# Optimization experiments

Hardware: AMD Instinct MI355X
Metric: run time of the kernel (lower is better)

The kernel has to match this reference:

```python
import jax, jax.numpy as jnp
import numpy as np

VAR_FLOOR = 0.002
BS, A, IN, H, L, NNH, ATT, NACT = 1024, 32, 96, 64, 16, 64, 32, 16


def _lin(x, w, b):
    return x @ w.T + b


def _lrelu(x):
    return jax.nn.leaky_relu(x, 0.01)


def setup_inputs() -> dict:
    key = jax.random.key(0)
    ks = jax.random.split(key, 24)
    def w(k, o, i):
        return jax.random.normal(k, (o, i), jnp.float32) / np.float32(np.sqrt(i))
    def b(k, o):
        return jax.random.normal(k, (o,), jnp.float32) * 0.01
    N = BS * A
    return {
        "inputs": jax.random.normal(ks[0], (N, IN), jnp.float32),
        "hidden_state": jax.random.normal(ks[1], (N, H), jnp.float32),
        "eps": jax.random.normal(ks[2], (N, A * L), jnp.float32),
        "fc1_w": w(ks[3], H, IN), "fc1_b": b(ks[4], H),
        "gru_wih": w(ks[5], 3 * H, H), "gru_whh": w(ks[6], 3 * H, H),
        "gru_bih": b(ks[7], 3 * H), "gru_bhh": b(ks[8], 3 * H),
        "fc2_w": w(ks[9], NACT, H), "fc2_b": b(ks[10], NACT),
        "emb_w1": w(ks[11], NNH, H), "emb_b1": b(ks[12], NNH),
        "bn_g": jnp.ones((NNH,), jnp.float32), "bn_b": jnp.zeros((NNH,), jnp.float32),
        "emb_w2": w(ks[13], A * L * 2, NNH), "emb_b2": b(ks[14], A * L * 2),
        "msg_w1": w(ks[15], NNH, H + L), "msg_b1": b(ks[16], NNH),
        "msg_w2": w(ks[17], NACT, NNH), "msg_b2": b(ks[18], NACT),
        "wq_w": w(ks[19], ATT, H), "wq_b": b(ks[20], ATT),
        "wk_w": w(ks[21], ATT, L), "wk_b": b(ks[22], ATT),
        "bs": BS, "t": 0,
    }


def reference(inputs, hidden_state, eps, fc1_w, fc1_b, gru_wih, gru_whh, gru_bih,
              gru_bhh, fc2_w, fc2_b, emb_w1, emb_b1, bn_g, bn_b, emb_w2, emb_b2,
              msg_w1, msg_b1, msg_w2, msg_b2, wq_w, wq_b, wk_w, wk_b, bs, t):
    Hd = fc1_w.shape[0]
    x = jax.nn.relu(_lin(inputs, fc1_w, fc1_b))
    h_in = hidden_state.reshape(-1, Hd)
    # GRUCell
    gi = _lin(x, gru_wih, gru_bih)
    gh = _lin(h_in, gru_whh, gru_bhh)
    ir, iz, inn = jnp.split(gi, 3, axis=-1)
    hr, hz, hn = jnp.split(gh, 3, axis=-1)
    r = jax.nn.sigmoid(ir + hr)
    z = jax.nn.sigmoid(iz + hz)
    n = jnp.tanh(inn + r * hn)
    h = (1.0 - z) * n + z * h_in
    q = _lin(h, fc2_w, fc2_b)
    # embed_net: Linear -> BatchNorm(train) -> LeakyReLU -> Linear
    z1 = _lin(h, emb_w1, emb_b1)
    z1 = bn_g * (z1 - z1.mean(0)) / jnp.sqrt(z1.var(0) + 1e-5) + bn_b
    lat_par = _lin(_lrelu(z1), emb_w2, emb_b2)
    D = lat_par.shape[-1] // 2
    Ld = wk_w.shape[1]
    Ag = D // Ld
    mu = lat_par[:, :D]
    var = jnp.clip(jnp.exp(lat_par[:, D:]), VAR_FLOOR, None)
    latent = (mu + jnp.sqrt(var) * eps).reshape(bs, Ag, Ag, Ld)  # [b,i,j,L]
    # msg_net on (h of receiver j, latent[b,i,j])
    h3 = h.reshape(bs, Ag, Hd)
    h_rep = jnp.broadcast_to(h3[:, None, :, :], (bs, Ag, Ag, Hd))  # [b,i,j]=h[b,j]
    msg_in = jnp.concatenate([h_rep, latent], axis=-1)
    msg = _lin(_lrelu(_lin(msg_in, msg_w1, msg_b1)), msg_w2, msg_b2)  # (b,A,A,n_act)
    # attention gating
    att = wq_w.shape[0]
    query = _lin(h, wq_w, wq_b).reshape(bs, Ag, att) / np.float32(np.sqrt(att))
    key_ = _lin(latent, wk_w, wk_b)  # (b,A,A,att)
    alpha = jnp.einsum('bia,bija->bij', query, key_)
    alpha = jnp.where(jnp.eye(Ag, dtype=bool)[None], -1e9, alpha)
    alpha = jax.nn.softmax(alpha, axis=-1)
    agg = jnp.einsum('bij,bijn->bjn', alpha, msg)  # sum gated msgs over sender i
    return_q = q + agg.reshape(bs * Ag, -1)
    return (return_q, h)
```

## Files before the change

kernel.cpp:

```cpp
#include <hip/hip_runtime.h>
#include <math.h>

namespace {

constexpr int NROW = 32768;
constexpr int HDIM = 64;
constexpr int DH   = 512;

typedef __attribute__((ext_vector_type(8))) short bf16x8;
typedef __attribute__((ext_vector_type(4))) float f32x4;
typedef __attribute__((ext_vector_type(4))) unsigned uint4e;
typedef __attribute__((ext_vector_type(2))) unsigned uint2e;

__device__ __forceinline__ float sigmoidf_(float x) { return 1.f / (1.f + __expf(-x)); }
__device__ __forceinline__ float lrelu_(float x) { return x > 0.f ? x : 0.01f * x; }
__device__ __forceinline__ unsigned pkbf(float a, float b) {
  unsigned ua = __float_as_uint(a) + 0x8000u;
  unsigned ub = __float_as_uint(b) + 0x8000u;
  return __builtin_amdgcn_perm(ub, ua, 0x07060302);
}

__global__ __launch_bounds__(512, 1) void k_fgru(
    const float* __restrict__ in,
    const float* __restrict__ hprev,
    const float* __restrict__ fc1w, const float* __restrict__ fc1b,
    const float* __restrict__ wih, const float* __restrict__ whh,
    const float* __restrict__ bih, const float* __restrict__ bhh,
    float* __restrict__ hT, float* __restrict__ hout) {
  __shared__ char smem[73728];
  const int t = threadIdx.x;
  const int n0 = blockIdx.x * 128;
  short*    xS = (short*)smem;
  unsigned* gU = (unsigned*)(smem + 18432);
  float*    trF = (float*)(smem + 18432);

  const float2* wih2 = (const float2*)wih;
  const float2* whh2 = (const float2*)whh;
  {
    float2 wv[12];
#pragma unroll
    for (int i = 0; i < 12; ++i) {
      int idx = t + 512 * i;
      int row = idx >> 5, kp = idx & 31;
      wv[i] = wih2[row * 32 + kp];
    }
#pragma unroll
    for (int i = 0; i < 12; ++i) {
      int idx = t + 512 * i;
      int row = idx >> 5, kp = idx & 31;
      int gate = row >> 6, cl = row & 63;
      gU[(gate * 64 + cl) * 36 + kp] = pkbf(wv[i].x, wv[i].y);
    }
#pragma unroll
    for (int i = 0; i < 12; ++i) {
      int idx = t + 512 * i;
      int row = idx >> 5, kp = idx & 31;
      wv[i] = whh2[row * 32 + kp];
    }
#pragma unroll
    for (int i = 0; i < 12; ++i) {
      int idx = t + 512 * i;
      int row = idx >> 5, kp = idx & 31;
      int gate = row >> 6, cl = row & 63;
      gU[((gate + 3) * 64 + cl) * 36 + kp] = pkbf(wv[i].x, wv[i].y);
    }
  }

  const int w = t >> 6, l = t & 63;
  const int m = l & 15, g = l >> 4;
  const int rowA = n0 + w * 16 + m;

  bf16x8 af[3];
#pragma unroll
  for (int ks = 0; ks < 3; ++ks) {
    const float4* p = (const float4*)(in + (size_t)rowA * 96 + ks * 32 + g * 8);
    float4 a = p[0], b = p[1];
    union { unsigned u[4]; bf16x8 h; } tw;
    tw.u[0] = pkbf(a.x, a.y); tw.u[1] = pkbf(a.z, a.w);
    tw.u[2] = pkbf(b.x, b.y); tw.u[3] = pkbf(b.z, b.w);
    af[ks] = tw.h;
  }
  {
    f32x4 accx[4];
#pragma unroll
    for (int ct = 0; ct < 4; ++ct) accx[ct] = (f32x4){0.f, 0.f, 0.f, 0.f};
#pragma unroll
    for (int ct = 0; ct < 4; ++ct)
#pragma unroll
      for (int ks = 0; ks < 3; ++ks) {
        const float4* p = (const float4*)(fc1w + (ct * 16 + m) * 96 + ks * 32 + g * 8);
        float4 a = p[0], b = p[1];
        union { unsigned u[4]; bf16x8 h; } tw;
        tw.u[0] = pkbf(a.x, a.y); tw.u[1] = pkbf(a.z, a.w);
        tw.u[2] = pkbf(b.x, b.y); tw.u[3] = pkbf(b.z, b.w);
        accx[ct] = __builtin_amdgcn_mfma_f32_16x16x32_bf16(af[ks], tw.h, accx[ct], 0, 0, 0);
      }
#pragma unroll
    for (int ct = 0; ct < 4; ++ct) {
      int c = ct * 16 + m;
      float bc = fc1b[c];
#pragma unroll
      for (int reg = 0; reg < 4; ++reg) {
        int nl = w * 16 + g * 4 + reg;
        float v = fmaxf(accx[ct][reg] + bc, 0.f);
        xS[nl * 72 + c] = (short)((__float_as_uint(v) + 0x8000u) >> 16);
      }
    }
  }
  __syncthreads();

  bf16x8 ax[2], ah[2];
#pragma unroll
  for (int ks = 0; ks < 2; ++ks) {
    ax[ks] = *(const bf16x8*)(xS + (w * 16 + m) * 72 + ks * 32 + g * 8);
    const float4* p = (const float4*)(hprev + (size_t)rowA * 64 + ks * 32 + g * 8);
    float4 a = p[0], b = p[1];
    union { unsigned u[4]; bf16x8 h; } tw;
    tw.u[0] = pkbf(a.x, a.y); tw.u[1] = pkbf(a.z, a.w);
    tw.u[2] = pkbf(b.x, b.y); tw.u[3] = pkbf(b.z, b.w);
    ah[ks] = tw.h;
  }
  const short* gS = (const short*)gU;
  float hc[4][4];
#pragma unroll 1
  for (int ct = 0; ct < 4; ++ct) {
    f32x4 a_ir = (f32x4){0.f,0.f,0.f,0.f}, a_iz = (f32x4){0.f,0.f,0.f,0.f},
          a_in = (f32x4){0.f,0.f,0.f,0.f}, a_hr = (f32x4){0.f,0.f,0.f,0.f},
          a_hz = (f32x4){0.f,0.f,0.f,0.f}, a_hn = (f32x4){0.f,0.f,0.f,0.f};
    int crow = ct * 16 + m;
#pragma unroll
    for (int ks = 0; ks < 2; ++ks) {
      bf16x8 b0 = *(const bf16x8*)(gS + (0 * 64 + crow) * 72 + ks * 32 + g * 8);
      bf16x8 b1 = *(const bf16x8*)(gS + (1 * 64 + crow) * 72 + ks * 32 + g * 8);
      bf16x8 b2 = *(const bf16x8*)(gS + (2 * 64 + crow) * 72 + ks * 32 + g * 8);
      bf16x8 b3 = *(const bf16x8*)(gS + (3 * 64 + crow) * 72 + ks * 32 + g * 8);
      bf16x8 b4 = *(const bf16x8*)(gS + (4 * 64 + crow) * 72 + ks * 32 + g * 8);
      bf16x8 b5 = *(const bf16x8*)(gS + (5 * 64 + crow) * 72 + ks * 32 + g * 8);
      a_ir = __builtin_amdgcn_mfma_f32_16x16x32_bf16(ax[ks], b0, a_ir, 0, 0, 0);
      a_iz = __builtin_amdgcn_mfma_f32_16x16x32_bf16(ax[ks], b1, a_iz, 0, 0, 0);
      a_in = __builtin_amdgcn_mfma_f32_16x16x32_bf16(ax[ks], b2, a_in, 0, 0, 0);
      a_hr = __builtin_amdgcn_mfma_f32_16x16x32_bf16(ah[ks], b3, a_hr, 0, 0, 0);
      a_hz = __builtin_amdgcn_mfma_f32_16x16x32_bf16(ah[ks], b4, a_hz, 0, 0, 0);
      a_hn = __builtin_amdgcn_mfma_f32_16x16x32_bf16(ah[ks], b5, a_hn, 0, 0, 0);
    }
    float bir = bih[crow], biz = bih[64 + crow], bin = bih[128 + crow];
    float bhr = bhh[crow], bhz = bhh[64 + crow], bhn = bhh[128 + crow];
#pragma unroll
    for (int reg = 0; reg < 4; ++reg) {
      int nl = w * 16 + g * 4 + reg;
      float hv = hprev[(size_t)(n0 + nl) * 64 + crow];
      float r  = sigmoidf_(a_ir[reg] + bir + a_hr[reg] + bhr);
      float z  = sigmoidf_(a_iz[reg] + biz + a_hz[reg] + bhz);
      float nn = tanhf(a_in[reg] + bin + r * (a_hn[reg] + bhn));
      hc[ct][reg] = (1.f - z) * nn + z * hv;
    }
  }
  __syncthreads();
#pragma unroll
  for (int ct = 0; ct < 4; ++ct)
#pragma unroll
    for (int reg = 0; reg < 4; ++reg)
      trF[(ct * 16 + m) * 133 + w * 16 + g * 4 + reg] = hc[ct][reg];
  __syncthreads();
#pragma unroll
  for (int i = 0; i < 16; ++i) {
    int idx = t + 512 * i;
    int nl = idx & 127, cl = idx >> 7;
    hT[(size_t)cl * NROW + n0 + nl] = trF[cl * 133 + nl];
  }
#pragma unroll
  for (int i = 0; i < 16; ++i) {
    int idx = t + 512 * i;
    int c = idx & 63, nl = idx >> 6;
    hout[(size_t)(n0 + nl) * 64 + c] = trF[c * 133 + nl];
  }
}

__global__ __launch_bounds__(256) void k_heads(const float* __restrict__ hT,
    const float* __restrict__ fc2w, const float* __restrict__ fc2b,
    const float* __restrict__ wqw, const float* __restrict__ wkw,
    const float* __restrict__ ew1, const float* __restrict__ eb1,
    float* __restrict__ qT, float* __restrict__ qkT, float* __restrict__ z1T,
    float* __restrict__ part) {
  __shared__ char smem[36864];
  const int t = threadIdx.x;
  const int n0 = blockIdx.x * 128;
  unsigned* hU = (unsigned*)smem;
  unsigned* wU = (unsigned*)(smem + 18432);
  float* sp1 = (float*)(smem + 18432 + 13824);
  float* sp2 = sp1 + 256;
  const float qs = 0.17677669529663687f;

  {
    float va[16], vb[16];
#pragma unroll
    for (int i = 0; i < 16; ++i) {
      int idx = t + 256 * i;
      int nl = idx & 127, kp = idx >> 7;
      va[i] = hT[(size_t)(2 * kp) * NROW + n0 + nl];
      vb[i] = hT[(size_t)(2 * kp + 1) * NROW + n0 + nl];
    }
#pragma unroll
    for (int i = 0; i < 16; ++i) {
      int idx = t + 256 * i;
      int nl = idx & 127, kp = idx >> 7;
      hU[nl * 36 + kp] = pkbf(va[i], vb[i]);
    }
  }
  {
    float2 wv[10];
#pragma unroll
    for (int i = 0; i < 10; ++i) {
      int idx = t + 256 * i;
      int kp = idx & 31, cl = idx >> 5;
      const float* src = (cl < 16) ? (fc2w + cl * 64) : (ew1 + (cl - 16) * 64);
      wv[i] = *(const float2*)(src + 2 * kp);
    }
#pragma unroll
    for (int i = 0; i < 10; ++i) {
      int idx = t + 256 * i;
      int kp = idx & 31, cl = idx >> 5;
      int dst = (cl < 16) ? cl : (cl + 16);
      wU[dst * 36 + kp] = pkbf(wv[i].x, wv[i].y);
    }
  }
  {
    int kp = t & 31, ll = t >> 5;
#pragma unroll
    for (int h = 0; h < 2; ++h) {
      int row = ll + 8 * h;
      float s0 = 0.f, s1 = 0.f;
#pragma unroll
      for (int a = 0; a < 32; ++a) {
        float wk = wkw[a * 16 + row];
        s0 = fmaf(wk, wqw[a * 64 + 2 * kp], s0);
        s1 = fmaf(wk, wqw[a * 64 + 2 * kp + 1], s1);
      }
      wU[(16 + row) * 36 + kp] = pkbf(s0 * qs, s1 * qs);
    }
  }
  __syncthreads();

  const int w = t >> 6, l = t & 63;
  const int m = l & 15, g = l >> 4;
  const short* sH = (const short*)hU;
  const short* sW = (const short*)wU;

  bf16x8 af[2][2];
#pragma unroll
  for (int mt = 0; mt < 2; ++mt)
#pragma unroll
    for (int ks = 0; ks < 2; ++ks)
      af[mt][ks] = *(const bf16x8*)(sH + (w * 32 + mt * 16 + m) * 72 + ks * 32 + g * 8);

  f32x4 acc[2][6];
#pragma unroll
  for (int mt = 0; mt < 2; ++mt)
#pragma unroll
    for (int ct = 0; ct < 6; ++ct) acc[mt][ct] = (f32x4){0.f, 0.f, 0.f, 0.f};
#pragma unroll
  for (int ct = 0; ct < 6; ++ct)
#pragma unroll
    for (int ks = 0; ks < 2; ++ks) {
      bf16x8 bw = *(const bf16x8*)(sW + (ct * 16 + m) * 72 + ks * 32 + g * 8);
#pragma unroll
      for (int mt = 0; mt < 2; ++mt)
        acc[mt][ct] = __builtin_amdgcn_mfma_f32_16x16x32_bf16(af[mt][ks], bw, acc[mt][ct], 0, 0, 0);
    }

  float s1[4], s2[4];
#pragma unroll
  for (int zt = 0; zt < 4; ++zt) { s1[zt] = 0.f; s2[zt] = 0.f; }
#pragma unroll
  for (int mt = 0; mt < 2; ++mt) {
    int nb = n0 + w * 32 + mt * 16 + g * 4;
    {
      float bc = fc2b[m];
      f32x4 v;
#pragma unroll
      for (int reg = 0; reg < 4; ++reg) v[reg] = acc[mt][0][reg] + bc;
      *(f32x4*)(qT + (size_t)m * NROW + nb) = v;
    }
    *(f32x4*)(qkT + (size_t)m * NROW + nb) = acc[mt][1];
#pragma unroll
    for (int ct = 2; ct < 6; ++ct) {
      int z = (ct - 2) * 16 + m;
      float bc = eb1[z];
      f32x4 v;
#pragma unroll
      for (int reg = 0; reg < 4; ++reg) {
        float zv = acc[mt][ct][reg] + bc;
        v[reg] = zv;
        s1[ct - 2] += zv;
        s2[ct - 2] = fmaf(zv, zv, s2[ct - 2]);
      }
      *(f32x4*)(z1T + (size_t)z * NROW + nb) = v;
    }
  }
#pragma unroll
  for (int zt = 0; zt < 4; ++zt) {
    s1[zt] += __shfl_down(s1[zt], 16, 64);
    s1[zt] += __shfl_down(s1[zt], 32, 64);
    s2[zt] += __shfl_down(s2[zt], 16, 64);
    s2[zt] += __shfl_down(s2[zt], 32, 64);
  }
  if (l < 16) {
#pragma unroll
    for (int zt = 0; zt < 4; ++zt) {
      sp1[w * 64 + zt * 16 + m] = s1[zt];
      sp2[w * 64 + zt * 16 + m] = s2[zt];
    }
  }
  __syncthreads();
  if (t < 64) {
    float a1 = sp1[t] + sp1[64 + t] + sp1[128 + t] + sp1[192 + t];
    float a2 = sp2[t] + sp2[64 + t] + sp2[128 + t] + sp2[192 + t];
    part[(size_t)blockIdx.x * 128 + t] = a1;
    part[(size_t)blockIdx.x * 128 + 64 + t] = a2;
  }
}

__global__ void k_bnstat(const float* __restrict__ part,
    const float* __restrict__ bng, const float* __restrict__ bnb,
    float* __restrict__ stat) {
  int c = threadIdx.x;
  float s1 = 0.f, s2 = 0.f;
  for (int b = 0; b < 256; ++b) {
    s1 += part[(size_t)b * 128 + c];
    s2 += part[(size_t)b * 128 + 64 + c];
  }
  float mean = s1 * (1.f / NROW);
  float var = s2 * (1.f / NROW) - mean * mean;
  float rstd = rsqrtf(var + 1e-5f);
  float sc = bng[c] * rstd;
  stat[c] = sc;
  stat[64 + c] = bnb[c] - mean * sc;
}

__global__ __launch_bounds__(512, 1) void k_emb_gemm(const float* __restrict__ z1T,
    const float* __restrict__ stat,
    const float* __restrict__ ew2, const float* __restrict__ eb2,
    const float* __restrict__ eps,
    unsigned* __restrict__ latB16g) {
  __shared__ char smem[55296];
  const int t = threadIdx.x;
  const int n0 = blockIdx.x * 128;

  unsigned* aU = (unsigned*)smem;
  unsigned* wB0 = (unsigned*)(smem + 18432);
  unsigned* wB1 = (unsigned*)(smem + 36864);

  const int w = t >> 6, l = t & 63;
  const int m = l & 15, g = l >> 4;
  const float2* ew2_2 = (const float2*)ew2;
  const float stdfloor = 0.04472135955f;

  {
    float va[8], vb[8];
#pragma unroll
    for (int i = 0; i < 8; ++i) {
      int idx = t + 512 * i;
      int nl = idx & 127, kp = idx >> 7;
      va[i] = z1T[(size_t)(2 * kp) * NROW + n0 + nl];
      vb[i] = z1T[(size_t)(2 * kp + 1) * NROW + n0 + nl];
    }
#pragma unroll
    for (int i = 0; i < 8; ++i) {
      int idx = t + 512 * i;
      int nl = idx & 127, kp = idx >> 7;
      float v0 = lrelu_(fmaf(stat[2 * kp], va[i], stat[64 + 2 * kp]));
      float v1 = lrelu_(fmaf(stat[2 * kp + 1], vb[i], stat[64 + 2 * kp + 1]));
      aU[nl * 36 + kp] = pkbf(v0, v1);
    }
  }

  float2 wm[4], wl[4];
#pragma unroll
  for (int i = 0; i < 4; ++i) {
    int idx = t + 512 * i;
    int kp = idx & 31, cl = idx >> 5;
    wm[i] = ew2_2[(size_t)cl * 32 + kp];
    wl[i] = ew2_2[(size_t)(512 + cl) * 32 + kp];
  }
#pragma unroll
  for (int i = 0; i < 4; ++i) {
    int idx = t + 512 * i;
    int kp = idx & 31, cl = idx >> 5;
    wB0[cl * 36 + kp] = pkbf(wm[i].x, wm[i].y);
    wB0[(64 + cl) * 36 + kp] = pkbf(wl[i].x, wl[i].y);
  }
#pragma unroll
  for (int i = 0; i < 4; ++i) {
    int idx = t + 512 * i;
    int kp = idx & 31, cl = idx >> 5;
    wm[i] = ew2_2[(size_t)(64 + cl) * 32 + kp];
    wl[i] = ew2_2[(size_t)(512 + 64 + cl) * 32 + kp];
  }
  float epsC[16];
#pragma unroll
  for (int ct = 0; ct < 4; ++ct)
#pragma unroll
    for (int reg = 0; reg < 4; ++reg)
      epsC[ct * 4 + reg] =
          eps[(size_t)(n0 + w * 16 + g * 4 + reg) * 512 + ct * 16 + m];
  __syncthreads();

  const short* sA = (const short*)aU;
  bf16x8 af[2];
#pragma unroll
  for (int ks = 0; ks < 2; ++ks)
    af[ks] = *(const bf16x8*)(sA + (w * 16 + m) * 72 + ks * 32 + g * 8);

  const int rowG = n0 + w * 16 + g * 4;

#pragma unroll 1
  for (int cb = 0; cb < 8; ++cb) {
    const int c0 = cb * 64;
    unsigned* wbC = (cb & 1) ? wB1 : wB0;
    unsigned* wbN = (cb & 1) ? wB0 : wB1;

    if (cb < 7) {
#pragma unroll
      for (int i = 0; i < 4; ++i) {
        int idx = t + 512 * i;
        int kp = idx & 31, cl = idx >> 5;
        wbN[cl * 36 + kp] = pkbf(wm[i].x, wm[i].y);
        wbN[(64 + cl) * 36 + kp] = pkbf(wl[i].x, wl[i].y);
      }
    }
    if (cb < 6) {
      int c2 = (cb + 2) * 64;
#pragma unroll
      for (int i = 0; i < 4; ++i) {
        int idx = t + 512 * i;
        int kp = idx & 31, cl = idx >> 5;
        wm[i] = ew2_2[(size_t)(c2 + cl) * 32 + kp];
        wl[i] = ew2_2[(size_t)(512 + c2 + cl) * 32 + kp];
      }
    }
    float epsN[16];
    if (cb < 7) {
#pragma unroll
      for (int ct = 0; ct < 4; ++ct)
#pragma unroll
        for (int reg = 0; reg < 4; ++reg)
          epsN[ct * 4 + reg] =
              eps[(size_t)(rowG + reg) * 512 + c0 + 64 + ct * 16 + m];
    }

    const short* sW = (const short*)wbC;
    f32x4 accm[4], accl[4];
#pragma unroll
    for (int ct = 0; ct < 4; ++ct) {
      accm[ct] = (f32x4){0.f, 0.f, 0.f, 0.f};
      accl[ct] = (f32x4){0.f, 0.f, 0.f, 0.f};
    }
#pragma unroll
    for (int ct = 0; ct < 4; ++ct)
#pragma unroll
      for (int ks = 0; ks < 2; ++ks) {
        bf16x8 bm = *(const bf16x8*)(sW + (ct * 16 + m) * 72 + ks * 32 + g * 8);
        bf16x8 bl = *(const bf16x8*)(sW + (64 + ct * 16 + m) * 72 + ks * 32 + g * 8);
        accm[ct] = __builtin_amdgcn_mfma_f32_16x16x32_bf16(af[ks], bm, accm[ct], 0, 0, 0);
        accl[ct] = __builtin_amdgcn_mfma_f32_16x16x32_bf16(af[ks], bl, accl[ct], 0, 0, 0);
      }

#pragma unroll
    for (int ct = 0; ct < 4; ++ct) {
      int c = c0 + ct * 16 + m;
      float ebm = eb2[c], ebl = eb2[DH + c];
#pragma unroll
      for (int reg = 0; reg < 4; ++reg) {
        float mu = accm[ct][reg] + ebm;
        float lv = accl[ct][reg] + ebl;
        float sd = fmaxf(__expf(0.5f * lv), stdfloor);
        float lat = fmaf(sd, epsC[ct * 4 + reg], mu);
        float lat2 = __shfl_xor(lat, 1, 64);
        if (!(m & 1)) {
          latB16g[(size_t)(rowG + reg) * 256 + (c0 >> 1) + ct * 8 + (m >> 1)] =
              pkbf(lat, lat2);
        }
      }
    }
#pragma unroll
    for (int i2 = 0; i2 < 16; ++i2) epsC[i2] = epsN[i2];
    __syncthreads();
  }
}

constexpr int LATB_OFF = 0;
constexpr int H3B_OFF  = 40960;
constexpr int W1H_OFF  = 45568;
constexpr int W1L_OFF  = 54784;
constexpr int W2P_OFF  = 57344;
constexpr int ALL_OFF  = 59648;
constexpr int MT_OFF   = 63872;
constexpr int QKL_OFF  = 74112;
__global__ __launch_bounds__(256, 1) void k_msg(
    const unsigned* __restrict__ latB16g, const float* __restrict__ qkT,
    const float* __restrict__ qT, const float* __restrict__ hrow,
    const float* __restrict__ w1, const float* __restrict__ b1,
    const float* __restrict__ w2, const float* __restrict__ b2,
    float* __restrict__ out) {
  __shared__ char smem[76672];
  const int t = threadIdx.x;
  const int b = blockIdx.x;
  const int b32 = b * 32;
  unsigned* latB_dw = (unsigned*)(smem + LATB_OFF);

  {
    const uint4e* g4 = (const uint4e*)latB16g + (size_t)b32 * 64;
#pragma unroll
    for (int half = 0; half < 2; ++half) {
      uint4e v[4];
#pragma unroll
      for (int it = 0; it < 4; ++it) v[it] = g4[t + 256 * (4 * half + it)];
#pragma unroll
      for (int it = 0; it < 4; ++it) {
        int idx = t + 256 * (4 * half + it);
        int i = idx >> 6;
        int rem = idx & 63;
        int j = rem >> 1, hh = rem & 1;
        unsigned* dst = latB_dw + (i * 32 + j) * 10 + hh * 4;
        *(uint2e*)dst = (uint2e){v[it].x, v[it].y};
        *(uint2e*)(dst + 2) = (uint2e){v[it].z, v[it].w};
      }
    }
  }
  {
    float* qkL = (float*)(smem + QKL_OFF);
    int i = t & 31;
    float v0 = qkT[(size_t)((t >> 5)) * NROW + b32 + i];
    float v1 = qkT[(size_t)((t >> 5) + 8) * NROW + b32 + i];
    qkL[i * 20 + (t >> 5)] = v0;
    qkL[i * 20 + (t >> 5) + 8] = v1;
  }
  {
    int cp = t & 31, jj = t >> 5;
    const float2* h2 = (const float2*)hrow;
    float2 hv[4];
#pragma unroll
    for (int it = 0; it < 4; ++it)
      hv[it] = h2[((size_t)(b32 + jj + 8 * it) * 64 + 2 * cp) >> 1];
    unsigned* dst = (unsigned*)(smem + H3B_OFF);
#pragma unroll
    for (int it = 0; it < 4; ++it)
      dst[(jj + 8 * it) * 36 + cp] = pkbf(hv[it].x, hv[it].y);
  }
  {
    int kp = t & 31, cc = t >> 5;
    const float2* w12 = (const float2*)w1;
    float2 wv[8];
#pragma unroll
    for (int it = 0; it < 8; ++it)
      wv[it] = w12[((cc + 8 * it) * 80 + 2 * kp) >> 1];
    unsigned* dst = (unsigned*)(smem + W1H_OFF);
#pragma unroll
    for (int it = 0; it < 8; ++it)
      dst[(cc + 8 * it) * 36 + kp] = pkbf(wv[it].x, wv[it].y);
  }
  {
    int lp = t & 7, cc = t >> 3;
    const float2* w12 = (const float2*)w1;
    float2 wv[2];
#pragma unroll
    for (int it = 0; it < 2; ++it)
      wv[it] = w12[((cc + 32 * it) * 80 + 64 + 2 * lp) >> 1];
    unsigned* dst = (unsigned*)(smem + W1L_OFF);
#pragma unroll
    for (int it = 0; it < 2; ++it)
      dst[(cc + 32 * it) * 10 + lp] = pkbf(wv[it].x, wv[it].y);
  }
  {
    int pp = t & 31, nn = t >> 5;
    const float2* w22 = (const float2*)w2;
    int p = 2 * pp;
    int c = ((p >> 2) & 3) * 16 + (p >> 4) * 4 + (p & 3);
    float2 wv0 = w22[(nn * 64 + c) >> 1];
    float2 wv1 = w22[((nn + 8) * 64 + c) >> 1];
    unsigned* dst = (unsigned*)(smem + W2P_OFF);
    dst[nn * 36 + pp] = pkbf(wv0.x, wv0.y);
    dst[(nn + 8) * 36 + pp] = pkbf(wv1.x, wv1.y);
  }
  __syncthreads();

  {
    const float* qkL = (const float*)(smem + QKL_OFF);
    float* alL = (float*)(smem + ALL_OFF);
#pragma unroll 1
    for (int p = 0; p < 4; ++p) {
      int i = (t >> 5) + 8 * p;
      int j = t & 31;
      const unsigned* lr = latB_dw + (i * 32 + j) * 10;
      float acc = 0.f;
#pragma unroll
      for (int d = 0; d < 8; ++d) {
        unsigned u = lr[d];
        float lo = __uint_as_float(u << 16);
        float hi = __uint_as_float(u & 0xffff0000u);
        acc = fmaf(lo, qkL[i * 20 + 2 * d], acc);
        acc = fmaf(hi, qkL[i * 20 + 2 * d + 1], acc);
      }
      if (j == i) acc = -1e9f;
      float mx = acc;
#pragma unroll
      for (int msk = 16; msk > 0; msk >>= 1) mx = fmaxf(mx, __shfl_xor(mx, msk, 32));
      float e = __expf(acc - mx);
      float s = e;
#pragma unroll
      for (int msk = 16; msk > 0; msk >>= 1) s += __shfl_xor(s, msk, 32);
      alL[i * 33 + j] = e / s;
    }
  }

  const int w = t >> 6, l = t & 63;
  const int n15 = l & 15, q = l >> 4;
  const int jh = w & 1, ibase = (w >> 1) * 16;
  const bool kact = (q < 2);

  f32x4 hp[4];
#pragma unroll
  for (int ct = 0; ct < 4; ++ct) hp[ct] = (f32x4){0.f, 0.f, 0.f, 0.f};
#pragma unroll
  for (int ct = 0; ct < 4; ++ct)
#pragma unroll
    for (int ks = 0; ks < 2; ++ks) {
      bf16x8 aF = *(const bf16x8*)(smem + W1H_OFF + (ct * 16 + n15) * 144 + ks * 64 + q * 16);
      bf16x8 bF = *(const bf16x8*)(smem + H3B_OFF + (jh * 16 + n15) * 144 + ks * 64 + q * 16);
      hp[ct] = __builtin_amdgcn_mfma_f32_16x16x32_bf16(aF, bF, hp[ct], 0, 0, 0);
    }
#pragma unroll
  for (int ct = 0; ct < 4; ++ct)
#pragma unroll
    for (int reg = 0; reg < 4; ++reg)
      hp[ct][reg] += b1[ct * 16 + q * 4 + reg];

  bf16x8 aL[4];
#pragma unroll
  for (int ct = 0; ct < 4; ++ct) {
    union { unsigned u[4]; bf16x8 h; } tmp;
    tmp.u[0] = tmp.u[1] = tmp.u[2] = tmp.u[3] = 0u;
    if (kact) {
      const unsigned* p = (const unsigned*)(smem + W1L_OFF) + (ct * 16 + n15) * 10 + q * 4;
      uint2e d0 = *(const uint2e*)p;
      uint2e d1 = *(const uint2e*)(p + 2);
      tmp.u[0] = d0.x; tmp.u[1] = d0.y; tmp.u[2] = d1.x; tmp.u[3] = d1.y;
    }
    aL[ct] = tmp.h;
  }
  bf16x8 w2F[2];
#pragma unroll
  for (int ks = 0; ks < 2; ++ks)
    w2F[ks] = *(const bf16x8*)(smem + W2P_OFF + n15 * 144 + ks * 64 + q * 16);
  float b2v[4];
#pragma unroll
  for (int reg = 0; reg < 4; ++reg) b2v[reg] = b2[q * 4 + reg];

  __syncthreads();

  float agg[4] = {0.f, 0.f, 0.f, 0.f};
  char* wb = smem + MT_OFF + w * 2560;
  const float* alLf = (const float*)(smem + ALL_OFF);
#pragma unroll 1
  for (int it = 0; it < 16; ++it) {
    int ii = ibase + it;
    int r = ii * 32 + jh * 16 + n15;
    union { unsigned u[4]; bf16x8 h; } latF;
    latF.u[0] = latF.u[1] = latF.u[2] = latF.u[3] = 0u;
    if (kact) {
      const unsigned* p = latB_dw + r * 10 + q * 4;
      uint2e d0 = *(const uint2e*)p;
      uint2e d1 = *(const uint2e*)(p + 2);
      latF.u[0] = d0.x; latF.u[1] = d0.y; latF.u[2] = d1.x; latF.u[3] = d1.y;
    }
    f32x4 acc[4];
#pragma unroll
    for (int ct = 0; ct < 4; ++ct) {
      acc[ct] = (f32x4){0.f, 0.f, 0.f, 0.f};
      acc[ct] = __builtin_amdgcn_mfma_f32_16x16x32_bf16(aL[ct], latF.h, acc[ct], 0, 0, 0);
    }
#pragma unroll
    for (int h = 0; h < 2; ++h) {
      float m0[4], m1[4];
#pragma unroll
      for (int reg = 0; reg < 4; ++reg) {
        float v0 = acc[2 * h][reg] + hp[2 * h][reg];
        float v1 = acc[2 * h + 1][reg] + hp[2 * h + 1][reg];
        m0[reg] = fmaxf(v0, 0.01f * v0);
        m1[reg] = fmaxf(v1, 0.01f * v1);
      }
      uint4e pk4;
      pk4.x = pkbf(m0[0], m0[1]); pk4.y = pkbf(m0[2], m0[3]);
      pk4.z = pkbf(m1[0], m1[1]); pk4.w = pkbf(m1[2], m1[3]);
      int qp = (2 * q + h) & 3;
      *(uint4e*)(wb + (q >> 1) * 1280 + n15 * 80 + qp * 16) = pk4;
    }
    f32x4 msg = (f32x4){0.f, 0.f, 0.f, 0.f};
#pragma unroll
    for (int ks = 0; ks < 2; ++ks) {
      bf16x8 mF = *(const bf16x8*)(wb + ks * 1280 + n15 * 80 + q * 16);
      msg = __builtin_amdgcn_mfma_f32_16x16x32_bf16(w2F[ks], mF, msg, 0, 0, 0);
    }
    float aw = alLf[ii * 33 + jh * 16 + n15];
#pragma unroll
    for (int reg = 0; reg < 4; ++reg)
      agg[reg] = fmaf(aw, msg[reg] + b2v[reg], agg[reg]);
  }
  {
    f32x4 av; av[0] = agg[0]; av[1] = agg[1]; av[2] = agg[2]; av[3] = agg[3];
    *(f32x4*)(wb + n15 * 80 + q * 16) = av;
  }
  __syncthreads();
#pragma unroll
  for (int tt = 0; tt < 2; ++tt) {
    int idx = t + 256 * tt;
    int jg = idx >> 4, nn = idx & 15;
    int jh2 = jg >> 4, jl = jg & 15;
    float a0 = *(const float*)(smem + MT_OFF + jh2 * 2560 + jl * 80 + nn * 4);
    float a1 = *(const float*)(smem + MT_OFF + (jh2 + 2) * 2560 + jl * 80 + nn * 4);
    out[(size_t)b * 512 + idx] = a0 + a1 + qT[(size_t)nn * NROW + b32 + jg];
  }
}

}

extern "C" void kernel_launch(void* const* d_in, const int* in_sizes, int n_in,
                              void* d_out, int out_size, void* d_ws, size_t ws_size,
                              hipStream_t stream) {
  (void)in_sizes; (void)n_in; (void)out_size; (void)ws_size;
  const float* inputs = (const float*)d_in[0];
  const float* hidden = (const float*)d_in[1];
  const float* eps    = (const float*)d_in[2];
  const float* fc1w   = (const float*)d_in[3];
  const float* fc1b   = (const float*)d_in[4];
  const float* wih    = (const float*)d_in[5];
  const float* whh    = (const float*)d_in[6];
  const float* bih    = (const float*)d_in[7];
  const float* bhh    = (const float*)d_in[8];
  const float* fc2w   = (const float*)d_in[9];
  const float* fc2b   = (const float*)d_in[10];
  const float* ew1    = (const float*)d_in[11];
  const float* eb1    = (const float*)d_in[12];
  const float* bng    = (const float*)d_in[13];
  const float* bnb    = (const float*)d_in[14];
  const float* ew2    = (const float*)d_in[15];
  const float* eb2    = (const float*)d_in[16];
  const float* w1     = (const float*)d_in[17];
  const float* b1     = (const float*)d_in[18];
  const float* w2     = (const float*)d_in[19];
  const float* b2     = (const float*)d_in[20];
  const float* wqw    = (const float*)d_in[21];
  const float* wkw    = (const float*)d_in[23];

  float* ws = (float*)d_ws;
  float* hT     = ws;
  float* qT     = ws + 2097152;
  float* qkT    = ws + 2621440;
  float* z1T    = ws + 3670016;
  float* part   = ws + 5767168;
  float* stat   = ws + 5832704;
  unsigned* latB16g = (unsigned*)(ws + 5832832);

  float* out_q = (float*)d_out;
  float* out_h = (float*)d_out + 524288;

  hipLaunchKernelGGL(k_fgru, dim3(256), dim3(512), 0, stream,
                     inputs, hidden, fc1w, fc1b, wih, whh, bih, bhh, hT, out_h);
  hipLaunchKernelGGL(k_heads, dim3(256), dim3(256), 0, stream,
                     hT, fc2w, fc2b, wqw, wkw, ew1, eb1, qT, qkT, z1T, part);
  hipLaunchKernelGGL(k_bnstat, dim3(1), dim3(64), 0, stream, part, bng, bnb, stat);
  hipLaunchKernelGGL(k_emb_gemm, dim3(256), dim3(512), 0, stream, z1T, stat, ew2, eb2, eps, latB16g);
  hipLaunchKernelGGL(k_msg, dim3(1024), dim3(256), 0, stream,
                     latB16g, qkT, qT, out_h, w1, b1, w2, b2, out_q);
}
```

Baseline: 250.0 us.

## Stage full emb_w2 weight in LDS once and drop per-chunk double buffering

```diff
diff --git a/kernel.cpp b/kernel.cpp
--- a/kernel.cpp
+++ b/kernel.cpp
@@ -342,13 +342,11 @@
     const float* __restrict__ ew2, const float* __restrict__ eb2,
     const float* __restrict__ eps,
     unsigned* __restrict__ latB16g) {
-  __shared__ char smem[55296];
+  __shared__ char smem[161280];
   const int t = threadIdx.x;
   const int n0 = blockIdx.x * 128;
-
   unsigned* aU = (unsigned*)smem;
-  unsigned* wB0 = (unsigned*)(smem + 18432);
-  unsigned* wB1 = (unsigned*)(smem + 36864);
+  unsigned* wU = (unsigned*)(smem + 17920);
 
   const int w = t >> 6, l = t & 63;
   const int m = l & 15, g = l >> 4;
@@ -370,31 +368,26 @@
       int nl = idx & 127, kp = idx >> 7;
       float v0 = lrelu_(fmaf(stat[2 * kp], va[i], stat[64 + 2 * kp]));
       float v1 = lrelu_(fmaf(stat[2 * kp + 1], vb[i], stat[64 + 2 * kp + 1]));
-      aU[nl * 36 + kp] = pkbf(v0, v1);
-    }
-  }
-
-  float2 wm[4], wl[4];
-#pragma unroll
-  for (int i = 0; i < 4; ++i) {
-    int idx = t + 512 * i;
-    int kp = idx & 31, cl = idx >> 5;
-    wm[i] = ew2_2[(size_t)cl * 32 + kp];
-    wl[i] = ew2_2[(size_t)(512 + cl) * 32 + kp];
-  }
-#pragma unroll
-  for (int i = 0; i < 4; ++i) {
-    int idx = t + 512 * i;
-    int kp = idx & 31, cl = idx >> 5;
-    wB0[cl * 36 + kp] = pkbf(wm[i].x, wm[i].y);
-    wB0[(64 + cl) * 36 + kp] = pkbf(wl[i].x, wl[i].y);
-  }
-#pragma unroll
-  for (int i = 0; i < 4; ++i) {
-    int idx = t + 512 * i;
-    int kp = idx & 31, cl = idx >> 5;
-    wm[i] = ew2_2[(size_t)(64 + cl) * 32 + kp];
-    wl[i] = ew2_2[(size_t)(512 + 64 + cl) * 32 + kp];
+      aU[nl * 35 + kp] = pkbf(v0, v1);
+    }
+  }
+#pragma unroll 1
+  for (int rb = 0; rb < 4; ++rb) {
+    float2 wv[16];
+#pragma unroll
+    for (int j = 0; j < 16; ++j) {
+      int idx = t + 512 * (rb * 16 + j);
+      int kp = idx & 31, r = idx >> 5;
+      wv[j] = ew2_2[(size_t)r * 32 + kp];
+    }
+#pragma unroll
+    for (int j = 0; j < 16; ++j) {
+      int idx = t + 512 * (rb * 16 + j);
+      int kp = idx & 31, r = idx >> 5;
+      int chunk = (r >> 6) & 7;
+      int lrow = (r & 63) + ((r >> 9) << 6);
+      wU[chunk * 4480 + lrow * 35 + kp] = pkbf(wv[j].x, wv[j].y);
+    }
   }
   float epsC[16];
 #pragma unroll
@@ -409,35 +402,13 @@
   bf16x8 af[2];
 #pragma unroll
   for (int ks = 0; ks < 2; ++ks)
-    af[ks] = *(const bf16x8*)(sA + (w * 16 + m) * 72 + ks * 32 + g * 8);
+    af[ks] = *(const bf16x8*)(sA + (w * 16 + m) * 70 + ks * 32 + g * 8);
 
   const int rowG = n0 + w * 16 + g * 4;
 
 #pragma unroll 1
   for (int cb = 0; cb < 8; ++cb) {
     const int c0 = cb * 64;
-    unsigned* wbC = (cb & 1) ? wB1 : wB0;
-    unsigned* wbN = (cb & 1) ? wB0 : wB1;
-
-    if (cb < 7) {
-#pragma unroll
-      for (int i = 0; i < 4; ++i) {
-        int idx = t + 512 * i;
-        int kp = idx & 31, cl = idx >> 5;
-        wbN[cl * 36 + kp] = pkbf(wm[i].x, wm[i].y);
-        wbN[(64 + cl) * 36 + kp] = pkbf(wl[i].x, wl[i].y);
-      }
-    }
-    if (cb < 6) {
-      int c2 = (cb + 2) * 64;
-#pragma unroll
-      for (int i = 0; i < 4; ++i) {
-        int idx = t + 512 * i;
-        int kp = idx & 31, cl = idx >> 5;
-        wm[i] = ew2_2[(size_t)(c2 + cl) * 32 + kp];
-        wl[i] = ew2_2[(size_t)(512 + c2 + cl) * 32 + kp];
-      }
-    }
     float epsN[16];
     if (cb < 7) {
 #pragma unroll
@@ -448,7 +419,7 @@
               eps[(size_t)(rowG + reg) * 512 + c0 + 64 + ct * 16 + m];
     }
 
-    const short* sW = (const short*)wbC;
+    const short* sW = (const short*)(wU + cb * 4480);
     f32x4 accm[4], accl[4];
 #pragma unroll
     for (int ct = 0; ct < 4; ++ct) {
@@ -459,8 +430,8 @@
     for (int ct = 0; ct < 4; ++ct)
 #pragma unroll
       for (int ks = 0; ks < 2; ++ks) {
-        bf16x8 bm = *(const bf16x8*)(sW + (ct * 16 + m) * 72 + ks * 32 + g * 8);
-        bf16x8 bl = *(const bf16x8*)(sW + (64 + ct * 16 + m) * 72 + ks * 32 + g * 8);
+        bf16x8 bm = *(const bf16x8*)(sW + (ct * 16 + m) * 70 + ks * 32 + g * 8);
+        bf16x8 bl = *(const bf16x8*)(sW + (64 + ct * 16 + m) * 70 + ks * 32 + g * 8);
         accm[ct] = __builtin_amdgcn_mfma_f32_16x16x32_bf16(af[ks], bm, accm[ct], 0, 0, 0);
         accl[ct] = __builtin_amdgcn_mfma_f32_16x16x32_bf16(af[ks], bl, accl[ct], 0, 0, 0);
       }
@@ -484,7 +455,6 @@
     }
 #pragma unroll
     for (int i2 = 0; i2 < 16; ++i2) epsC[i2] = epsN[i2];
-    __syncthreads();
   }
 }
 
```

Result: slower. 258.7 us (+3.5%).
